# Kernel tuning notes

Hardware: AMD Instinct MI355X
Metric: run time of the kernel (lower is better)

The kernel has to match this reference:

```python
import jax, jax.numpy as jnp
import numpy as np

BATCH = 8192
FEATS = 4096
RATE = 0.1
ANNEAL = 0.5 + 0.1  # self.anneal = 0.5 + anneal


def setup_inputs() -> dict:
    key = jax.random.key(0)
    k1, k2 = jax.random.split(key)
    inputs = jax.random.normal(k1, (BATCH, FEATS), dtype=jnp.float32)
    # standard-normal draws, one per feature (replaces the serial map_fn RNG)
    noise = jax.random.normal(k2, (FEATS,), dtype=jnp.float32)
    return {"inputs": inputs, "noise": noise}


def reference(inputs, noise):
    # SegDropout (training path), agg_method='mean', noise_type='gaussian'
    F = inputs.shape[-1]
    x_agg = jnp.mean(inputs, axis=0)                      # [F] batch-wise aggregate
    x_min = jnp.min(x_agg)
    x_max = jnp.max(x_agg)
    # quantize each feature's aggregate into one of F+1 integer bins
    bins = (F * (x_agg - x_min) / (x_max - x_min)).astype(jnp.int32)  # [F], values in [0, F]
    # unique_with_counts + gather(counts, idx) == histogram lookup per feature
    counts_per_bin = jnp.bincount(bins, length=F + 1)      # [F+1]
    counts = counts_per_bin[bins].astype(inputs.dtype)     # [F] count of each feature's bin
    dr = RATE ** (1.0 / (ANNEAL * counts))                 # annealed per-bin dropout rate
    dr = jnp.where(counts == 1.0, jnp.asarray(RATE, inputs.dtype), dr)
    sigma = jnp.sqrt(dr / (1.0 - dr))                      # [F]
    # multiplicative Gaussian noise ~ N(1, sigma) per feature
    return inputs * (1.0 + sigma * noise)
```

## Files before the change

kernel.cpp:

```cpp
#include <hip/hip_runtime.h>

#define BATCH 8192
#define FEATS 4096


__global__ __launch_bounds__(256) void colsum_kernel(const float* __restrict__ in,
                                                     double* __restrict__ sums) {
    const int colBase = blockIdx.x * 1024 + threadIdx.x * 4;
    const int rowsPerBlk = BATCH / gridDim.y;
    const int row0 = blockIdx.y * rowsPerBlk;
    const float4* p = (const float4*)in + (size_t)row0 * (FEATS / 4) + (colBase >> 2);
    double a0 = 0.0, a1 = 0.0, a2 = 0.0, a3 = 0.0;
    for (int r = 0; r < rowsPerBlk; ++r) {
        float4 v = p[(size_t)r * (FEATS / 4)];
        a0 += (double)v.x; a1 += (double)v.y; a2 += (double)v.z; a3 += (double)v.w;
    }
    atomicAdd(&sums[colBase + 0], a0);
    atomicAdd(&sums[colBase + 1], a1);
    atomicAdd(&sums[colBase + 2], a2);
    atomicAdd(&sums[colBase + 3], a3);
}

__global__ __launch_bounds__(1024) void config_kernel(const double* __restrict__ sums,
                                                      const float* __restrict__ noise,
                                                      float* __restrict__ scale) {
    __shared__ double s_mean[FEATS];
    __shared__ double s_red[1024];
    __shared__ unsigned s_hist[FEATS + 1];
    const int tid = threadIdx.x;

    double lmin = 1e300, lmax = -1e300;
    for (int k = 0; k < 4; ++k) {
        int c = tid + k * 1024;
        double m = sums[c] * (1.0 / (double)BATCH);
        s_mean[c] = m;
        lmin = fmin(lmin, m);
        lmax = fmax(lmax, m);
    }
    s_red[tid] = lmin; __syncthreads();
    for (int s = 512; s > 0; s >>= 1) {
        if (tid < s) s_red[tid] = fmin(s_red[tid], s_red[tid + s]);
        __syncthreads();
    }
    const double xmin = s_red[0]; __syncthreads();
    s_red[tid] = lmax; __syncthreads();
    for (int s = 512; s > 0; s >>= 1) {
        if (tid < s) s_red[tid] = fmax(s_red[tid], s_red[tid + s]);
        __syncthreads();
    }
    const double xmax = s_red[0]; __syncthreads();

    for (int i = tid; i < FEATS + 1; i += 1024) s_hist[i] = 0;
    __syncthreads();

    int binr[4];
    const double denom = xmax - xmin;
    for (int k = 0; k < 4; ++k) {
        int c = tid + k * 1024;
        double b = ((double)FEATS * (s_mean[c] - xmin)) / denom;
        int bi = (int)b;
        binr[k] = bi;
        atomicAdd(&s_hist[bi], 1u);
    }
    __syncthreads();

    for (int k = 0; k < 4; ++k) {
        int c = tid + k * 1024;
        unsigned cnt = s_hist[binr[k]];
        double dr = (cnt == 1u) ? 0.1 : pow(0.1, 1.0 / (0.6 * (double)cnt));
        double sg = sqrt(dr / (1.0 - dr));
        scale[c] = (float)(1.0 + sg * (double)noise[c]);
    }
}

__global__ __launch_bounds__(256) void scale_kernel(const float4* __restrict__ in,
                                                    const float4* __restrict__ scale,
                                                    float4* __restrict__ out, int n4) {
    int idx = blockIdx.x * 256 + threadIdx.x;
    int stride = gridDim.x * 256;
    for (int i = idx; i < n4; i += stride) {
        float4 v = in[i];
        float4 s = scale[i & (FEATS / 4 - 1)];
        v.x *= s.x; v.y *= s.y; v.z *= s.z; v.w *= s.w;
        out[i] = v;
    }
}

extern "C" void kernel_launch(void* const* d_in, const int* in_sizes, int n_in,
                              void* d_out, int out_size, void* d_ws, size_t ws_size,
                              hipStream_t stream) {
    const float* in = (const float*)d_in[0];
    const float* noise = (const float*)d_in[1];
    float* out = (float*)d_out;
    double* sums = (double*)d_ws;
    float* scale = (float*)(sums + FEATS);

    hipMemsetAsync(d_ws, 0, FEATS * sizeof(double), stream);

    dim3 g1(4, 128);
    colsum_kernel<<<g1, 256, 0, stream>>>(in, sums);
    config_kernel<<<1, 1024, 0, stream>>>(sums, noise, scale);
    scale_kernel<<<2048, 256, 0, stream>>>((const float4*)in, (const float4*)scale,
                                           (float4*)out, BATCH * FEATS / 4);
}
```

Baseline: 274.3 us.

## Replace atomic column sums with partial buffers and a separate reduce kernel

```diff
diff --git a/kernel.cpp b/kernel.cpp
--- a/kernel.cpp
+++ b/kernel.cpp
@@ -2,26 +2,35 @@
 
 #define BATCH 8192
 #define FEATS 4096
+#define CHUNKS 128
+#define ROWS_PER_CHUNK (BATCH / CHUNKS)
 
 
-__global__ __launch_bounds__(256) void colsum_kernel(const float* __restrict__ in,
-                                                     double* __restrict__ sums) {
+__global__ __launch_bounds__(256) void colsum_part(const float* __restrict__ in,
+                                                   double* __restrict__ partials) {
     const int colBase = blockIdx.x * 1024 + threadIdx.x * 4;
-    const int rowsPerBlk = BATCH / gridDim.y;
-    const int row0 = blockIdx.y * rowsPerBlk;
+    const int row0 = blockIdx.y * ROWS_PER_CHUNK;
     const float4* p = (const float4*)in + (size_t)row0 * (FEATS / 4) + (colBase >> 2);
     double a0 = 0.0, a1 = 0.0, a2 = 0.0, a3 = 0.0;
-    for (int r = 0; r < rowsPerBlk; ++r) {
+#pragma unroll 8
+    for (int r = 0; r < ROWS_PER_CHUNK; ++r) {
         float4 v = p[(size_t)r * (FEATS / 4)];
         a0 += (double)v.x; a1 += (double)v.y; a2 += (double)v.z; a3 += (double)v.w;
     }
-    atomicAdd(&sums[colBase + 0], a0);
-    atomicAdd(&sums[colBase + 1], a1);
-    atomicAdd(&sums[colBase + 2], a2);
-    atomicAdd(&sums[colBase + 3], a3);
+    double* dst = partials + (size_t)blockIdx.y * FEATS + colBase;
+    dst[0] = a0; dst[1] = a1; dst[2] = a2; dst[3] = a3;
 }
 
-__global__ __launch_bounds__(1024) void config_kernel(const double* __restrict__ sums,
+__global__ __launch_bounds__(256) void reduce_mean(const double* __restrict__ partials,
+                                                   double* __restrict__ means) {
+    const int c = blockIdx.x * 256 + threadIdx.x;
+    double s = 0.0;
+#pragma unroll 8
+    for (int k = 0; k < CHUNKS; ++k) s += partials[(size_t)k * FEATS + c];
+    means[c] = s * (1.0 / (double)BATCH);
+}
+
+__global__ __launch_bounds__(1024) void config_kernel(const double* __restrict__ means,
                                                       const float* __restrict__ noise,
                                                       float* __restrict__ scale) {
     __shared__ double s_mean[FEATS];
@@ -30,9 +39,10 @@
     const int tid = threadIdx.x;
 
     double lmin = 1e300, lmax = -1e300;
+#pragma unroll
     for (int k = 0; k < 4; ++k) {
         int c = tid + k * 1024;
-        double m = sums[c] * (1.0 / (double)BATCH);
+        double m = means[c];
         s_mean[c] = m;
         lmin = fmin(lmin, m);
         lmax = fmax(lmax, m);
@@ -55,6 +65,7 @@
 
     int binr[4];
     const double denom = xmax - xmin;
+#pragma unroll
     for (int k = 0; k < 4; ++k) {
         int c = tid + k * 1024;
         double b = ((double)FEATS * (s_mean[c] - xmin)) / denom;
@@ -64,10 +75,12 @@
     }
     __syncthreads();
 
+    const double K = -2.302585092994045684017991454684364208;
+#pragma unroll
     for (int k = 0; k < 4; ++k) {
         int c = tid + k * 1024;
         unsigned cnt = s_hist[binr[k]];
-        double dr = (cnt == 1u) ? 0.1 : pow(0.1, 1.0 / (0.6 * (double)cnt));
+        double dr = (cnt == 1u) ? 0.1 : exp(K / (0.6 * (double)cnt));
         double sg = sqrt(dr / (1.0 - dr));
         scale[c] = (float)(1.0 + sg * (double)noise[c]);
     }
@@ -75,15 +88,12 @@
 
 __global__ __launch_bounds__(256) void scale_kernel(const float4* __restrict__ in,
                                                     const float4* __restrict__ scale,
-                                                    float4* __restrict__ out, int n4) {
-    int idx = blockIdx.x * 256 + threadIdx.x;
-    int stride = gridDim.x * 256;
-    for (int i = idx; i < n4; i += stride) {
-        float4 v = in[i];
-        float4 s = scale[i & (FEATS / 4 - 1)];
-        v.x *= s.x; v.y *= s.y; v.z *= s.z; v.w *= s.w;
-        out[i] = v;
-    }
+                                                    float4* __restrict__ out) {
+    const int i = blockIdx.x * 256 + threadIdx.x;
+    float4 v = in[i];
+    float4 s = scale[i & (FEATS / 4 - 1)];
+    v.x *= s.x; v.y *= s.y; v.z *= s.z; v.w *= s.w;
+    out[i] = v;
 }
 
 extern "C" void kernel_launch(void* const* d_in, const int* in_sizes, int n_in,
@@ -92,14 +102,14 @@
     const float* in = (const float*)d_in[0];
     const float* noise = (const float*)d_in[1];
     float* out = (float*)d_out;
-    double* sums = (double*)d_ws;
-    float* scale = (float*)(sums + FEATS);
+    double* partials = (double*)d_ws;
+    double* means = partials + (size_t)CHUNKS * FEATS;
+    float* scale = (float*)(means + FEATS);
 
-    hipMemsetAsync(d_ws, 0, FEATS * sizeof(double), stream);
-
-    dim3 g1(4, 128);
-    colsum_kernel<<<g1, 256, 0, stream>>>(in, sums);
-    config_kernel<<<1, 1024, 0, stream>>>(sums, noise, scale);
-    scale_kernel<<<2048, 256, 0, stream>>>((const float4*)in, (const float4*)scale,
-                                           (float4*)out, BATCH * FEATS / 4);
+    dim3 g1(4, CHUNKS);
+    colsum_part<<<g1, 256, 0, stream>>>(in, partials);
+    reduce_mean<<<FEATS / 256, 256, 0, stream>>>(partials, means);
+    config_kernel<<<1, 1024, 0, stream>>>(means, noise, scale);
+    scale_kernel<<<BATCH * FEATS / 4 / 256, 256, 0, stream>>>(
+        (const float4*)in, (const float4*)scale, (float4*)out);
 }
```

Result: faster. 260.0 us (-5.2%).
